# Kernel tuning notes

Measured on AMD Instinct MI355X. Metric: run time of the kernel, lower is better.

## Reference

```python
import jax, jax.numpy as jnp
import numpy as np

B, L, D, N, K = 4, 4096, 1024, 64, 3
EPS = 1e-6

def setup_inputs() -> dict:
    key = jax.random.key(0)
    ks = jax.random.split(key, 24)
    f32 = jnp.float32
    inp = {
        'T': jax.random.normal(ks[0], (B, L, D), f32),
        'norm_scale': jnp.ones((D,), f32),
        'in_w': jax.random.normal(ks[1], (2 * D, D), f32) * (1.0 / np.sqrt(D)),
        'in_b': jnp.zeros((2 * D,), f32),
        'dw_w': jax.random.normal(ks[2], (D, 1, K), f32) * (1.0 / np.sqrt(K)),
        'dw_b': jnp.zeros((D,), f32),
        'pw_w': jax.random.normal(ks[3], (D, D), f32) * (1.0 / np.sqrt(D)),
        'pw_b': jnp.zeros((D,), f32),
        'f_win': jax.random.normal(ks[4], (N, D), f32) * (1.0 / np.sqrt(D)),
        'f_wout': jax.random.normal(ks[5], (D, N), f32) * (1.0 / np.sqrt(N)),
        'f_logA': jax.random.normal(ks[6], (N,), f32) * 0.02,
        'f_B': jax.random.normal(ks[7], (N,), f32) * 0.02,
        'f_C': jax.random.normal(ks[8], (N,), f32) * 0.02,
        'f_logdt': jnp.array(0.0, f32),
        'b_win': jax.random.normal(ks[9], (N, D), f32) * (1.0 / np.sqrt(D)),
        'b_wout': jax.random.normal(ks[10], (D, N), f32) * (1.0 / np.sqrt(N)),
        'b_logA': jax.random.normal(ks[11], (N,), f32) * 0.02,
        'b_B': jax.random.normal(ks[12], (N,), f32) * 0.02,
        'b_C': jax.random.normal(ks[13], (N,), f32) * 0.02,
        'b_logdt': jnp.array(0.0, f32),
        'out_w': jax.random.normal(ks[14], (D, D), f32) * (1.0 / np.sqrt(D)),
        'out_b': jnp.zeros((D,), f32),
    }
    return inp

def _ssm(x, win, wout, logA, Bp, Cp, logdt):
    # ZOH discretization of diagonal SSM
    dt = jnp.exp(logdt)
    A = -jnp.exp(logA)
    Abar = jnp.exp(A * dt)
    denom = jnp.where(jnp.abs(A) < EPS, jnp.ones_like(A), A)
    frac = jnp.where(jnp.abs(A) < EPS, dt, (Abar - 1.0) / denom)
    Bbar = frac * Bp
    u = jnp.einsum('bld,nd->bln', x, win)  # (B,L,N)
    h0 = jnp.zeros((x.shape[0], win.shape[0]), x.dtype)
    def step(h, ut):
        h = h * Abar + ut * Bbar
        return h, h * Cp
    _, ys = jax.lax.scan(step, h0, jnp.swapaxes(u, 0, 1))  # (L,B,N)
    y = jnp.swapaxes(ys, 0, 1)
    return jnp.einsum('bln,dn->bld', y, wout)

def reference(T, norm_scale, in_w, in_b, dw_w, dw_b, pw_w, pw_b,
              f_win, f_wout, f_logA, f_B, f_C, f_logdt,
              b_win, b_wout, b_logA, b_B, b_C, b_logdt,
              out_w, out_b):
    # RMSNorm
    rms = jnp.sqrt(jnp.mean(T * T, axis=-1, keepdims=True) + EPS)
    Tn = T / rms * norm_scale
    # in_linear -> chunk
    xz = Tn @ in_w.T + in_b
    x, z = jnp.split(xz, 2, axis=-1)
    gate = jax.nn.sigmoid(z)
    # depthwise-separable conv1d (NCH layout)
    xc = jnp.swapaxes(x, 1, 2)  # (B,D,L)
    xc = jax.lax.conv_general_dilated(
        xc, dw_w, window_strides=(1,), padding=[(K // 2, K // 2)],
        dimension_numbers=('NCH', 'OIH', 'NCH'), feature_group_count=D)
    xc = xc + dw_b[None, :, None]
    xc = jnp.einsum('bdl,ed->bel', xc, pw_w) + pw_b[None, :, None]
    x_conv = jnp.swapaxes(xc, 1, 2)  # (B,L,D)
    # bidirectional SSM
    y_f = _ssm(x_conv, f_win, f_wout, f_logA, f_B, f_C, f_logdt)
    y_b = _ssm(jnp.flip(x_conv, axis=1), b_win, b_wout, b_logA, b_B, b_C, b_logdt)
    y_b = jnp.flip(y_b, axis=1)
    y = (y_f + y_b) * gate
    y = y @ out_w.T + out_b
    return T + y
```

## Files before the change

kernel.cpp:

```cpp
#include <hip/hip_runtime.h>
#include <cstdint>


#define L_SEQ 4096
#define D_DIM 1024
#define B_SZ 4
#define M_TOK (B_SZ * L_SEQ)
#define CHUNKS 64
#define CLEN (L_SEQ / CHUNKS)

typedef short bf16x8 __attribute__((ext_vector_type(8)));
typedef float floatx4 __attribute__((ext_vector_type(4)));

__device__ inline unsigned short f2bf(float f) {
  union { float f; unsigned int u; } v; v.f = f;
  unsigned int r = v.u + 0x7FFFu + ((v.u >> 16) & 1u);
  return (unsigned short)(r >> 16);
}
__device__ inline float bf2f(unsigned short h) {
  union { unsigned int u; float f; } v; v.u = ((unsigned int)h) << 16;
  return v.f;
}

__device__ inline void load_lds16(const unsigned short* g, unsigned short* l) {
  __builtin_amdgcn_global_load_lds(
      (const __attribute__((address_space(1))) unsigned int*)g,
      (__attribute__((address_space(3))) unsigned int*)l, 16, 0, 0);
}

__global__ __launch_bounds__(256) void rmsnorm_kernel(
    const float* __restrict__ T, const float* __restrict__ scale,
    unsigned short* __restrict__ Tn) {
  int tok = blockIdx.x;
  int t = threadIdx.x;
  const float4* row = (const float4*)(T + (size_t)tok * D_DIM);
  float4 v = row[t];
  float ss = v.x*v.x + v.y*v.y + v.z*v.z + v.w*v.w;
  #pragma unroll
  for (int off = 32; off > 0; off >>= 1) ss += __shfl_down(ss, off);
  __shared__ float part[4];
  if ((t & 63) == 0) part[t >> 6] = ss;
  __syncthreads();
  float total = part[0] + part[1] + part[2] + part[3];
  float rinv = rsqrtf(total * (1.0f / D_DIM) + 1e-6f);
  const float4* sc4 = (const float4*)scale;
  float4 s = sc4[t];
  ushort4 o;
  o.x = f2bf(v.x * rinv * s.x); o.y = f2bf(v.y * rinv * s.y);
  o.z = f2bf(v.z * rinv * s.z); o.w = f2bf(v.w * rinv * s.w);
  ((ushort4*)(Tn + (size_t)tok * D_DIM))[t] = o;
}

__global__ __launch_bounds__(256) void f2bf_vec_kernel(
    const float* __restrict__ in, unsigned short* __restrict__ out, int n4) {
  int i = blockIdx.x * 256 + threadIdx.x;
  if (i < n4) {
    float4 v = ((const float4*)in)[i];
    ushort4 o; o.x = f2bf(v.x); o.y = f2bf(v.y); o.z = f2bf(v.z); o.w = f2bf(v.w);
    ((ushort4*)out)[i] = o;
  }
}

__global__ void prepack_wy_kernel(
    const float* __restrict__ f_wout, const float* __restrict__ b_wout,
    unsigned short* __restrict__ Wy) {
  int i = blockIdx.x * blockDim.x + threadIdx.x;
  if (i < 128 * D_DIM) {
    int d = i >> 7, kk = i & 127;
    Wy[i] = f2bf((kk < 64) ? f_wout[d * 64 + kk] : b_wout[d * 64 + (kk - 64)]);
  }
}

__global__ void prepack_wu_kernel(
    const float* __restrict__ f_win, const float* __restrict__ b_win,
    unsigned short* __restrict__ Wu) {
  int i = blockIdx.x * blockDim.x + threadIdx.x;
  if (i < 128 * D_DIM) {
    int n = i >> 10, k = i & (D_DIM - 1);
    Wu[i] = f2bf((n < 64) ? f_win[n * D_DIM + k] : b_win[(n - 64) * D_DIM + k]);
  }
}

__global__ __launch_bounds__(256) void transpose_pw_kernel(
    const float* __restrict__ in, unsigned short* __restrict__ outT) {
  __shared__ float tile[32][33];
  int bd = blockIdx.x * 32, be = blockIdx.y * 32;
  int tx = threadIdx.x & 31, ty = threadIdx.x >> 5;
  #pragma unroll
  for (int j = 0; j < 32; j += 8)
    tile[ty + j][tx] = in[(size_t)(be + ty + j) * D_DIM + bd + tx];
  __syncthreads();
  #pragma unroll
  for (int j = 0; j < 32; j += 8)
    outT[(size_t)(bd + ty + j) * D_DIM + be + tx] = f2bf(tile[tx][ty + j]);
}

__global__ __launch_bounds__(64) void cbias_kernel(
    const float* __restrict__ f_win, const float* __restrict__ b_win,
    const float* __restrict__ pw_b, float* __restrict__ cb) {
  int n = blockIdx.x, t = threadIdx.x;
  const float* wrow = (n < 64) ? (f_win + (size_t)n * D_DIM)
                               : (b_win + (size_t)(n - 64) * D_DIM);
  float s = 0.0f;
  for (int e = t; e < D_DIM; e += 64) s += wrow[e] * pw_b[e];
  #pragma unroll
  for (int off = 32; off > 0; off >>= 1) s += __shfl_down(s, off);
  if (t == 0) cb[n] = s;
}

template<int MODE, typename OUT_T>
__global__ __launch_bounds__(256) void gemm_mfma_kernel(
    const unsigned short* __restrict__ A, const unsigned short* __restrict__ Bw,
    const float* __restrict__ bias, OUT_T* __restrict__ out,
    int M, int N, int Kt,
    const void* __restrict__ aux0, unsigned short* __restrict__ aux1) {
  __shared__ unsigned short As[2][128 * 32];
  __shared__ unsigned short Bs[2][128 * 32];
  int tid = threadIdx.x;
  int wave = tid >> 6, lane = tid & 63;
  int quad = lane >> 4, lrow = lane & 15;
  int nx = N >> 7;
  int nwg = nx * (M >> 7);
  int obid = blockIdx.y * nx + blockIdx.x;
  int swz = (nwg & 7) ? obid : ((obid & 7) * (nwg >> 3) + (obid >> 3));
  int bm = (swz / nx) << 7, bn = (swz % nx) << 7;
  int wm = (wave & 1) * 64, wn = (wave >> 1) * 64;

  int r0 = tid >> 2;
  int c8 = (tid & 3) * 8;
  const unsigned short* Ag0 = A  + (size_t)(bm + r0) * Kt + c8;
  const unsigned short* Ag1 = A  + (size_t)(bm + 64 + r0) * Kt + c8;
  const unsigned short* Bg0 = Bw + (size_t)(bn + r0) * Kt + c8;
  const unsigned short* Bg1 = Bw + (size_t)(bn + 64 + r0) * Kt + c8;
  int woff = wave * 512;

  floatx4 acc[4][4] = {};
  int nt = Kt >> 5;

  load_lds16(Ag0, &As[0][0] + woff);
  load_lds16(Ag1, &As[0][0] + 2048 + woff);
  load_lds16(Bg0, &Bs[0][0] + woff);
  load_lds16(Bg1, &Bs[0][0] + 2048 + woff);
  __syncthreads();

  int cur = 0;
  for (int t = 0; t < nt; ++t) {
    if (t + 1 < nt) {
      int k0 = (t + 1) << 5;
      int nb = cur ^ 1;
      load_lds16(Ag0 + k0, &As[nb][0] + woff);
      load_lds16(Ag1 + k0, &As[nb][0] + 2048 + woff);
      load_lds16(Bg0 + k0, &Bs[nb][0] + woff);
      load_lds16(Bg1 + k0, &Bs[nb][0] + 2048 + woff);
    }
    {
      const unsigned short* Ab = &As[cur][0];
      const unsigned short* Bb = &Bs[cur][0];
      bf16x8 af[4], bfr[4];
      #pragma unroll
      for (int mi = 0; mi < 4; ++mi)
        af[mi] = *(const bf16x8*)(Ab + (wm + mi * 16 + lrow) * 32 + quad * 8);
      #pragma unroll
      for (int ni = 0; ni < 4; ++ni)
        bfr[ni] = *(const bf16x8*)(Bb + (wn + ni * 16 + lrow) * 32 + quad * 8);
      __builtin_amdgcn_s_setprio(1);
      #pragma unroll
      for (int mi = 0; mi < 4; ++mi)
        #pragma unroll
        for (int ni = 0; ni < 4; ++ni)
          acc[mi][ni] = __builtin_amdgcn_mfma_f32_16x16x32_bf16(
              af[mi], bfr[ni], acc[mi][ni], 0, 0, 0);
      __builtin_amdgcn_s_setprio(0);
    }
    if (t + 1 < nt) {
      __syncthreads();
      cur ^= 1;
    }
  }

  #pragma unroll
  for (int mi = 0; mi < 4; ++mi) {
    #pragma unroll
    for (int ni = 0; ni < 4; ++ni) {
      #pragma unroll
      for (int r = 0; r < 4; ++r) {
        int m = bm + wm + mi * 16 + quad * 4 + r;
        int n = bn + wn + ni * 16 + lrow;
        float v = acc[mi][ni][r];
        if (MODE == 0) {
          if (bias) v += bias[n];
          if (sizeof(OUT_T) == 2) out[(size_t)m * N + n] = (OUT_T)f2bf(v);
          else                    out[(size_t)m * N + n] = (OUT_T)v;
        } else if (MODE == 1) {
          if (bias) v += bias[n];
          if (n < D_DIM) ((unsigned short*)out)[(size_t)m * D_DIM + n] = f2bf(v);
          else aux1[(size_t)m * D_DIM + (n - D_DIM)] = f2bf(1.0f / (1.0f + __expf(-v)));
        } else if (MODE == 2) {
          v *= bf2f(((const unsigned short*)aux0)[(size_t)m * N + n]);
          ((unsigned short*)out)[(size_t)m * N + n] = f2bf(v);
        } else {
          if (bias) v += bias[n];
          v += ((const float*)aux0)[(size_t)m * N + n];
          ((float*)out)[(size_t)m * N + n] = v;
        }
      }
    }
  }
}

__global__ __launch_bounds__(256) void dwconv_kernel(
    const unsigned short* __restrict__ x, const float* __restrict__ w,
    const float* __restrict__ b, unsigned short* __restrict__ out) {
  size_t i8 = (size_t)blockIdx.x * 256 + threadIdx.x;
  int d8 = (int)(i8 & (D_DIM / 8 - 1));
  size_t tok = i8 >> 7;
  int l = (int)(tok & (L_SEQ - 1));
  int d0 = d8 * 8;
  size_t base = tok * D_DIM + d0;
  bf16x8 cur = *(const bf16x8*)(x + base);
  float acc[8];
  #pragma unroll
  for (int j = 0; j < 8; ++j) {
    int d = d0 + j;
    acc[j] = b[d] + w[d * 3 + 1] * bf2f((unsigned short)cur[j]);
  }
  if (l > 0) {
    bf16x8 prv = *(const bf16x8*)(x + base - D_DIM);
    #pragma unroll
    for (int j = 0; j < 8; ++j) acc[j] += w[(d0 + j) * 3 + 0] * bf2f((unsigned short)prv[j]);
  }
  if (l < L_SEQ - 1) {
    bf16x8 nxt = *(const bf16x8*)(x + base + D_DIM);
    #pragma unroll
    for (int j = 0; j < 8; ++j) acc[j] += w[(d0 + j) * 3 + 2] * bf2f((unsigned short)nxt[j]);
  }
  bf16x8 o;
  #pragma unroll
  for (int j = 0; j < 8; ++j) o[j] = (short)f2bf(acc[j]);
  *(bf16x8*)(out + base) = o;
}

__device__ inline void ssm_params(
    int col,
    const float* f_logA, const float* f_B, const float* f_C, const float* f_logdt,
    const float* b_logA, const float* b_B, const float* b_C, const float* b_logdt,
    float& Abar, float& Bbar, float& Cc, float& Aa, float& dt) {
  int dir = col >> 6, n = col & 63;
  const float* logA  = dir ? b_logA  : f_logA;
  const float* Bp    = dir ? b_B     : f_B;
  const float* Cp    = dir ? b_C     : f_C;
  const float* logdt = dir ? b_logdt : f_logdt;
  dt = expf(logdt[0]);
  Aa = -expf(logA[n]);
  Abar = expf(Aa * dt);
  float frac = (fabsf(Aa) < 1e-6f) ? dt : (Abar - 1.0f) / Aa;
  Bbar = frac * Bp[n];
  Cc = Cp[n];
}

__global__ __launch_bounds__(128) void scan_s1_kernel(
    const float* __restrict__ u, float* __restrict__ states,
    const float* __restrict__ f_logA, const float* __restrict__ f_B,
    const float* __restrict__ f_C, const float* __restrict__ f_logdt,
    const float* __restrict__ b_logA, const float* __restrict__ b_B,
    const float* __restrict__ b_C, const float* __restrict__ b_logdt) {
  int col = threadIdx.x;
  int chunk = blockIdx.x, b = blockIdx.y;
  float Abar, Bbar, Cc, Aa, dt;
  ssm_params(col, f_logA, f_B, f_C, f_logdt, b_logA, b_B, b_C, b_logdt,
             Abar, Bbar, Cc, Aa, dt);
  size_t base = ((size_t)b * L_SEQ + (size_t)chunk * CLEN) * 128 + col;
  float h = 0.0f;
  if (col < 64) {
    for (int i0 = 0; i0 < CLEN; i0 += 8) {
      float uv[8];
      #pragma unroll
      for (int j = 0; j < 8; ++j) uv[j] = u[base + (size_t)(i0 + j) * 128];
      #pragma unroll
      for (int j = 0; j < 8; ++j) h = h * Abar + uv[j] * Bbar;
    }
  } else {
    for (int i0 = CLEN - 1; i0 >= 0; i0 -= 8) {
      float uv[8];
      #pragma unroll
      for (int j = 0; j < 8; ++j) uv[j] = u[base + (size_t)(i0 - j) * 128];
      #pragma unroll
      for (int j = 0; j < 8; ++j) h = h * Abar + uv[j] * Bbar;
    }
  }
  states[((size_t)b * CHUNKS + chunk) * 128 + col] = h;
}

__global__ __launch_bounds__(512) void scan_s2_kernel(
    const float* __restrict__ states, float* __restrict__ carries,
    const float* __restrict__ f_logA, const float* __restrict__ f_B,
    const float* __restrict__ f_C, const float* __restrict__ f_logdt,
    const float* __restrict__ b_logA, const float* __restrict__ b_B,
    const float* __restrict__ b_C, const float* __restrict__ b_logdt) {
  int tid = threadIdx.x;
  int b = tid >> 7, col = tid & 127;
  float Abar, Bbar, Cc, Aa, dt;
  ssm_params(col, f_logA, f_B, f_C, f_logdt, b_logA, b_B, b_C, b_logdt,
             Abar, Bbar, Cc, Aa, dt);
  float Ac = expf(Aa * dt * (float)CLEN);
  size_t sb = (size_t)b * CHUNKS * 128 + col;
  float cur = 0.0f;
  if (col < 64) {
    for (int c = 0; c < CHUNKS; ++c) {
      carries[sb + (size_t)c * 128] = cur;
      cur = cur * Ac + states[sb + (size_t)c * 128];
    }
  } else {
    for (int c = CHUNKS - 1; c >= 0; --c) {
      carries[sb + (size_t)c * 128] = cur;
      cur = cur * Ac + states[sb + (size_t)c * 128];
    }
  }
}

__global__ __launch_bounds__(128) void scan_s3_kernel(
    const float* __restrict__ u, const float* __restrict__ carries,
    unsigned short* __restrict__ y,
    const float* __restrict__ f_logA, const float* __restrict__ f_B,
    const float* __restrict__ f_C, const float* __restrict__ f_logdt,
    const float* __restrict__ b_logA, const float* __restrict__ b_B,
    const float* __restrict__ b_C, const float* __restrict__ b_logdt) {
  int col = threadIdx.x;
  int chunk = blockIdx.x, b = blockIdx.y;
  float Abar, Bbar, Cc, Aa, dt;
  ssm_params(col, f_logA, f_B, f_C, f_logdt, b_logA, b_B, b_C, b_logdt,
             Abar, Bbar, Cc, Aa, dt);
  size_t base = ((size_t)b * L_SEQ + (size_t)chunk * CLEN) * 128 + col;
  float h = carries[((size_t)b * CHUNKS + chunk) * 128 + col];
  if (col < 64) {
    for (int i0 = 0; i0 < CLEN; i0 += 8) {
      float uv[8];
      #pragma unroll
      for (int j = 0; j < 8; ++j) uv[j] = u[base + (size_t)(i0 + j) * 128];
      #pragma unroll
      for (int j = 0; j < 8; ++j) {
        h = h * Abar + uv[j] * Bbar;
        y[base + (size_t)(i0 + j) * 128] = f2bf(h * Cc);
      }
    }
  } else {
    for (int i0 = CLEN - 1; i0 >= 0; i0 -= 8) {
      float uv[8];
      #pragma unroll
      for (int j = 0; j < 8; ++j) uv[j] = u[base + (size_t)(i0 - j) * 128];
      #pragma unroll
      for (int j = 0; j < 8; ++j) {
        h = h * Abar + uv[j] * Bbar;
        y[base + (size_t)(i0 - j) * 128] = f2bf(h * Cc);
      }
    }
  }
}

extern "C" void kernel_launch(void* const* d_in, const int* in_sizes, int n_in,
                              void* d_out, int out_size, void* d_ws, size_t ws_size,
                              hipStream_t stream) {
  const float* T         = (const float*)d_in[0];
  const float* norm_scale= (const float*)d_in[1];
  const float* in_w      = (const float*)d_in[2];
  const float* in_b      = (const float*)d_in[3];
  const float* dw_w      = (const float*)d_in[4];
  const float* dw_b      = (const float*)d_in[5];
  const float* pw_w      = (const float*)d_in[6];
  const float* pw_b      = (const float*)d_in[7];
  const float* f_win     = (const float*)d_in[8];
  const float* f_wout    = (const float*)d_in[9];
  const float* f_logA    = (const float*)d_in[10];
  const float* f_B       = (const float*)d_in[11];
  const float* f_C       = (const float*)d_in[12];
  const float* f_logdt   = (const float*)d_in[13];
  const float* b_win     = (const float*)d_in[14];
  const float* b_wout    = (const float*)d_in[15];
  const float* b_logA    = (const float*)d_in[16];
  const float* b_B       = (const float*)d_in[17];
  const float* b_C       = (const float*)d_in[18];
  const float* b_logdt   = (const float*)d_in[19];
  const float* out_w     = (const float*)d_in[20];
  const float* out_b     = (const float*)d_in[21];
  float* out = (float*)d_out;

  char* ws = (char*)d_ws;
  const size_t MD = (size_t)M_TOK * D_DIM;
  unsigned short* gate  = (unsigned short*)ws;              ws += MD * 2;
  unsigned short* bufA  = (unsigned short*)ws;              ws += MD * 2;
  unsigned short* bufB  = (unsigned short*)ws;              ws += MD * 2;
  float*          u     = (float*)ws;                       ws += (size_t)M_TOK * 128 * 4;
  unsigned short* ybuf  = (unsigned short*)ws;              ws += (size_t)M_TOK * 128 * 2;
  unsigned short* w_in  = (unsigned short*)ws;              ws += (size_t)2 * D_DIM * D_DIM * 2;
  unsigned short* w_out = (unsigned short*)ws;              ws += (size_t)D_DIM * D_DIM * 2;
  unsigned short* pwT   = (unsigned short*)ws;              ws += (size_t)D_DIM * D_DIM * 2;
  unsigned short* Wu    = (unsigned short*)ws;              ws += (size_t)128 * D_DIM * 2;
  unsigned short* Wf    = (unsigned short*)ws;              ws += (size_t)128 * D_DIM * 2;
  unsigned short* Wy    = (unsigned short*)ws;              ws += (size_t)128 * D_DIM * 2;
  float*          cb    = (float*)ws;                       ws += 128 * 4;
  float*          states= (float*)ws;                       ws += (size_t)B_SZ * CHUNKS * 128 * 4;
  float*          carries=(float*)ws;

  f2bf_vec_kernel<<<(2 * D_DIM * D_DIM / 4 + 255) / 256, 256, 0, stream>>>(in_w, w_in, 2 * D_DIM * D_DIM / 4);
  f2bf_vec_kernel<<<(D_DIM * D_DIM / 4 + 255) / 256, 256, 0, stream>>>(out_w, w_out, D_DIM * D_DIM / 4);
  prepack_wy_kernel<<<(128 * D_DIM) / 256, 256, 0, stream>>>(f_wout, b_wout, Wy);
  prepack_wu_kernel<<<(128 * D_DIM) / 256, 256, 0, stream>>>(f_win, b_win, Wu);
  {
    dim3 g(D_DIM / 32, D_DIM / 32);
    transpose_pw_kernel<<<g, 256, 0, stream>>>(pw_w, pwT);
  }
  cbias_kernel<<<128, 64, 0, stream>>>(f_win, b_win, pw_b, cb);
  {
    dim3 g(D_DIM / 128, 1);
    gemm_mfma_kernel<0, unsigned short><<<g, 256, 0, stream>>>(
        Wu, pwT, nullptr, Wf, 128, D_DIM, D_DIM, nullptr, nullptr);
  }
  rmsnorm_kernel<<<M_TOK, 256, 0, stream>>>(T, norm_scale, bufA);
  {
    dim3 g((2 * D_DIM) / 128, M_TOK / 128);
    gemm_mfma_kernel<1, unsigned short><<<g, 256, 0, stream>>>(
        bufA, w_in, in_b, bufB, M_TOK, 2 * D_DIM, D_DIM, nullptr, gate);
  }
  dwconv_kernel<<<(MD / 8) / 256, 256, 0, stream>>>(bufB, dw_w, dw_b, bufA);
  {
    dim3 g(1, M_TOK / 128);
    gemm_mfma_kernel<0, float><<<g, 256, 0, stream>>>(
        bufA, Wf, cb, u, M_TOK, 128, D_DIM, nullptr, nullptr);
  }
  {
    dim3 g1(CHUNKS, B_SZ);
    scan_s1_kernel<<<g1, 128, 0, stream>>>(u, states, f_logA, f_B, f_C, f_logdt,
                                           b_logA, b_B, b_C, b_logdt);
    scan_s2_kernel<<<1, 512, 0, stream>>>(states, carries, f_logA, f_B, f_C, f_logdt,
                                          b_logA, b_B, b_C, b_logdt);
    scan_s3_kernel<<<g1, 128, 0, stream>>>(u, carries, ybuf, f_logA, f_B, f_C, f_logdt,
                                           b_logA, b_B, b_C, b_logdt);
  }
  {
    dim3 g(D_DIM / 128, M_TOK / 128);
    gemm_mfma_kernel<2, unsigned short><<<g, 256, 0, stream>>>(
        ybuf, Wy, nullptr, bufA, M_TOK, D_DIM, 128, gate, nullptr);
  }
  {
    dim3 g(D_DIM / 128, M_TOK / 128);
    gemm_mfma_kernel<3, float><<<g, 256, 0, stream>>>(
        bufA, w_out, out_b, out, M_TOK, D_DIM, D_DIM, T, nullptr);
  }
}
```

Baseline: 569.6 us.

## Split scan into more chunks, fully unroll chunk loops, merge weight prepack kernels

Raises the number of scan chunks per sequence from 64 to 512, so each chunk holds 8 steps. This gives the chunk-local scan kernels far more blocks, which are now fully unrolled with all loads issued up front. The carry-propagation kernel becomes longer (512 sequential steps), so it is batched with 8-wide prefetched loads to hide latency. The two weight-prepack kernels are merged into one launch. The trade-off is a longer serial pass and a larger state buffer in exchange for much more parallelism in the chunk passes.

Result: slower. 585.8 us (+2.8%).

```diff
diff --git a/kernel.cpp b/kernel.cpp
--- a/kernel.cpp
+++ b/kernel.cpp
@@ -6,7 +6,7 @@
 #define D_DIM 1024
 #define B_SZ 4
 #define M_TOK (B_SZ * L_SEQ)
-#define CHUNKS 64
+#define CHUNKS 512
 #define CLEN (L_SEQ / CHUNKS)
 
 typedef short bf16x8 __attribute__((ext_vector_type(8)));
@@ -61,23 +61,16 @@
   }
 }
 
-__global__ void prepack_wy_kernel(
+__global__ void prepack_w_kernel(
+    const float* __restrict__ f_win, const float* __restrict__ b_win,
     const float* __restrict__ f_wout, const float* __restrict__ b_wout,
-    unsigned short* __restrict__ Wy) {
-  int i = blockIdx.x * blockDim.x + threadIdx.x;
-  if (i < 128 * D_DIM) {
-    int d = i >> 7, kk = i & 127;
-    Wy[i] = f2bf((kk < 64) ? f_wout[d * 64 + kk] : b_wout[d * 64 + (kk - 64)]);
-  }
-}
-
-__global__ void prepack_wu_kernel(
-    const float* __restrict__ f_win, const float* __restrict__ b_win,
-    unsigned short* __restrict__ Wu) {
+    unsigned short* __restrict__ Wu, unsigned short* __restrict__ Wy) {
   int i = blockIdx.x * blockDim.x + threadIdx.x;
   if (i < 128 * D_DIM) {
     int n = i >> 10, k = i & (D_DIM - 1);
     Wu[i] = f2bf((n < 64) ? f_win[n * D_DIM + k] : b_win[(n - 64) * D_DIM + k]);
+    int d = i >> 7, kk = i & 127;
+    Wy[i] = f2bf((kk < 64) ? f_wout[d * 64 + kk] : b_wout[d * 64 + (kk - 64)]);
   }
 }
 
@@ -271,22 +264,17 @@
              Abar, Bbar, Cc, Aa, dt);
   size_t base = ((size_t)b * L_SEQ + (size_t)chunk * CLEN) * 128 + col;
   float h = 0.0f;
+  float uv[CLEN];
   if (col < 64) {
-    for (int i0 = 0; i0 < CLEN; i0 += 8) {
-      float uv[8];
-      #pragma unroll
-      for (int j = 0; j < 8; ++j) uv[j] = u[base + (size_t)(i0 + j) * 128];
-      #pragma unroll
-      for (int j = 0; j < 8; ++j) h = h * Abar + uv[j] * Bbar;
-    }
+    #pragma unroll
+    for (int j = 0; j < CLEN; ++j) uv[j] = u[base + (size_t)j * 128];
+    #pragma unroll
+    for (int j = 0; j < CLEN; ++j) h = h * Abar + uv[j] * Bbar;
   } else {
-    for (int i0 = CLEN - 1; i0 >= 0; i0 -= 8) {
-      float uv[8];
-      #pragma unroll
-      for (int j = 0; j < 8; ++j) uv[j] = u[base + (size_t)(i0 - j) * 128];
-      #pragma unroll
-      for (int j = 0; j < 8; ++j) h = h * Abar + uv[j] * Bbar;
-    }
+    #pragma unroll
+    for (int j = 0; j < CLEN; ++j) uv[j] = u[base + (size_t)(CLEN - 1 - j) * 128];
+    #pragma unroll
+    for (int j = 0; j < CLEN; ++j) h = h * Abar + uv[j] * Bbar;
   }
   states[((size_t)b * CHUNKS + chunk) * 128 + col] = h;
 }
@@ -306,14 +294,26 @@
   size_t sb = (size_t)b * CHUNKS * 128 + col;
   float cur = 0.0f;
   if (col < 64) {
-    for (int c = 0; c < CHUNKS; ++c) {
-      carries[sb + (size_t)c * 128] = cur;
-      cur = cur * Ac + states[sb + (size_t)c * 128];
+    for (int c0 = 0; c0 < CHUNKS; c0 += 8) {
+      float sv[8];
+      #pragma unroll
+      for (int j = 0; j < 8; ++j) sv[j] = states[sb + (size_t)(c0 + j) * 128];
+      #pragma unroll
+      for (int j = 0; j < 8; ++j) {
+        carries[sb + (size_t)(c0 + j) * 128] = cur;
+        cur = cur * Ac + sv[j];
+      }
     }
   } else {
-    for (int c = CHUNKS - 1; c >= 0; --c) {
-      carries[sb + (size_t)c * 128] = cur;
-      cur = cur * Ac + states[sb + (size_t)c * 128];
+    for (int c0 = CHUNKS - 1; c0 >= 0; c0 -= 8) {
+      float sv[8];
+      #pragma unroll
+      for (int j = 0; j < 8; ++j) sv[j] = states[sb + (size_t)(c0 - j) * 128];
+      #pragma unroll
+      for (int j = 0; j < 8; ++j) {
+        carries[sb + (size_t)(c0 - j) * 128] = cur;
+        cur = cur * Ac + sv[j];
+      }
     }
   }
 }
@@ -332,27 +332,22 @@
              Abar, Bbar, Cc, Aa, dt);
   size_t base = ((size_t)b * L_SEQ + (size_t)chunk * CLEN) * 128 + col;
   float h = carries[((size_t)b * CHUNKS + chunk) * 128 + col];
+  float uv[CLEN];
   if (col < 64) {
-    for (int i0 = 0; i0 < CLEN; i0 += 8) {
-      float uv[8];
-      #pragma unroll
-      for (int j = 0; j < 8; ++j) uv[j] = u[base + (size_t)(i0 + j) * 128];
-      #pragma unroll
-      for (int j = 0; j < 8; ++j) {
-        h = h * Abar + uv[j] * Bbar;
-        y[base + (size_t)(i0 + j) * 128] = f2bf(h * Cc);
-      }
+    #pragma unroll
+    for (int j = 0; j < CLEN; ++j) uv[j] = u[base + (size_t)j * 128];
+    #pragma unroll
+    for (int j = 0; j < CLEN; ++j) {
+      h = h * Abar + uv[j] * Bbar;
+      y[base + (size_t)j * 128] = f2bf(h * Cc);
     }
   } else {
-    for (int i0 = CLEN - 1; i0 >= 0; i0 -= 8) {
-      float uv[8];
-      #pragma unroll
-      for (int j = 0; j < 8; ++j) uv[j] = u[base + (size_t)(i0 - j) * 128];
-      #pragma unroll
-      for (int j = 0; j < 8; ++j) {
-        h = h * Abar + uv[j] * Bbar;
-        y[base + (size_t)(i0 - j) * 128] = f2bf(h * Cc);
-      }
+    #pragma unroll
+    for (int j = 0; j < CLEN; ++j) uv[j] = u[base + (size_t)(CLEN - 1 - j) * 128];
+    #pragma unroll
+    for (int j = 0; j < CLEN; ++j) {
+      h = h * Abar + uv[j] * Bbar;
+      y[base + (size_t)(CLEN - 1 - j) * 128] = f2bf(h * Cc);
     }
   }
 }
@@ -403,8 +398,7 @@
 
   f2bf_vec_kernel<<<(2 * D_DIM * D_DIM / 4 + 255) / 256, 256, 0, stream>>>(in_w, w_in, 2 * D_DIM * D_DIM / 4);
   f2bf_vec_kernel<<<(D_DIM * D_DIM / 4 + 255) / 256, 256, 0, stream>>>(out_w, w_out, D_DIM * D_DIM / 4);
-  prepack_wy_kernel<<<(128 * D_DIM) / 256, 256, 0, stream>>>(f_wout, b_wout, Wy);
-  prepack_wu_kernel<<<(128 * D_DIM) / 256, 256, 0, stream>>>(f_win, b_win, Wu);
+  prepack_w_kernel<<<(128 * D_DIM) / 256, 256, 0, stream>>>(f_win, b_win, f_wout, b_wout, Wu, Wy);
   {
     dim3 g(D_DIM / 32, D_DIM / 32);
     transpose_pw_kernel<<<g, 256, 0, stream>>>(pw_w, pwT);
```

## Split u-projection GEMM over K into two partial sums reduced in scan

Applied to the files above, without the earlier changes.

The N=128 projection GEMM (M=16384, K=1024) previously launched only 128 blocks, too few to fill the GPU. It now splits K into two halves with a dedicated double-buffered MFMA kernel, giving 256 blocks that each write a partial fp32 result. The two partials plus the bias are summed inside the scan kernels when u is read. The two weight prepack kernels are also merged into one launch. The cost is twice the u buffer memory and extra reads in both scan passes.

Result: no change. 566.4 us (-0.6%).

```diff
diff --git a/kernel.cpp b/kernel.cpp
--- a/kernel.cpp
+++ b/kernel.cpp
@@ -61,23 +61,16 @@
   }
 }
 
-__global__ void prepack_wy_kernel(
+__global__ void prepack_w_kernel(
+    const float* __restrict__ f_win, const float* __restrict__ b_win,
     const float* __restrict__ f_wout, const float* __restrict__ b_wout,
-    unsigned short* __restrict__ Wy) {
-  int i = blockIdx.x * blockDim.x + threadIdx.x;
-  if (i < 128 * D_DIM) {
-    int d = i >> 7, kk = i & 127;
-    Wy[i] = f2bf((kk < 64) ? f_wout[d * 64 + kk] : b_wout[d * 64 + (kk - 64)]);
-  }
-}
-
-__global__ void prepack_wu_kernel(
-    const float* __restrict__ f_win, const float* __restrict__ b_win,
-    unsigned short* __restrict__ Wu) {
+    unsigned short* __restrict__ Wu, unsigned short* __restrict__ Wy) {
   int i = blockIdx.x * blockDim.x + threadIdx.x;
   if (i < 128 * D_DIM) {
     int n = i >> 10, k = i & (D_DIM - 1);
     Wu[i] = f2bf((n < 64) ? f_win[n * D_DIM + k] : b_win[(n - 64) * D_DIM + k]);
+    int d = i >> 7, kk = i & 127;
+    Wy[i] = f2bf((kk < 64) ? f_wout[d * 64 + kk] : b_wout[d * 64 + (kk - 64)]);
   }
 }
 
@@ -208,6 +201,86 @@
   }
 }
 
+__global__ __launch_bounds__(256) void gemm_uproj_kernel(
+    const unsigned short* __restrict__ A, const unsigned short* __restrict__ Bw,
+    float* __restrict__ uP) {
+  __shared__ unsigned short As[2][128 * 32];
+  __shared__ unsigned short Bs[2][128 * 32];
+  int tid = threadIdx.x;
+  int wave = tid >> 6, lane = tid & 63;
+  int quad = lane >> 4, lrow = lane & 15;
+  int kh = blockIdx.x;
+  int bm = blockIdx.y * 128;
+  int wm = (wave & 1) * 64, wn = (wave >> 1) * 64;
+
+  int r0 = tid >> 2;
+  int c8 = (tid & 3) * 8;
+  int kbase = kh * 512;
+  const unsigned short* Ag0 = A  + (size_t)(bm + r0) * D_DIM + kbase + c8;
+  const unsigned short* Ag1 = A  + (size_t)(bm + 64 + r0) * D_DIM + kbase + c8;
+  const unsigned short* Bg0 = Bw + (size_t)(r0) * D_DIM + kbase + c8;
+  const unsigned short* Bg1 = Bw + (size_t)(64 + r0) * D_DIM + kbase + c8;
+  int woff = wave * 512;
+
+  floatx4 acc[4][4] = {};
+  const int nt = 512 >> 5;
+
+  load_lds16(Ag0, &As[0][0] + woff);
+  load_lds16(Ag1, &As[0][0] + 2048 + woff);
+  load_lds16(Bg0, &Bs[0][0] + woff);
+  load_lds16(Bg1, &Bs[0][0] + 2048 + woff);
+  __syncthreads();
+
+  int cur = 0;
+  for (int t = 0; t < nt; ++t) {
+    if (t + 1 < nt) {
+      int k0 = (t + 1) << 5;
+      int nb = cur ^ 1;
+      load_lds16(Ag0 + k0, &As[nb][0] + woff);
+      load_lds16(Ag1 + k0, &As[nb][0] + 2048 + woff);
+      load_lds16(Bg0 + k0, &Bs[nb][0] + woff);
+      load_lds16(Bg1 + k0, &Bs[nb][0] + 2048 + woff);
+    }
+    {
+      const unsigned short* Ab = &As[cur][0];
+      const unsigned short* Bb = &Bs[cur][0];
+      bf16x8 af[4], bfr[4];
+      #pragma unroll
+      for (int mi = 0; mi < 4; ++mi)
+        af[mi] = *(const bf16x8*)(Ab + (wm + mi * 16 + lrow) * 32 + quad * 8);
+      #pragma unroll
+      for (int ni = 0; ni < 4; ++ni)
+        bfr[ni] = *(const bf16x8*)(Bb + (wn + ni * 16 + lrow) * 32 + quad * 8);
+      __builtin_amdgcn_s_setprio(1);
+      #pragma unroll
+      for (int mi = 0; mi < 4; ++mi)
+        #pragma unroll
+        for (int ni = 0; ni < 4; ++ni)
+          acc[mi][ni] = __builtin_amdgcn_mfma_f32_16x16x32_bf16(
+              af[mi], bfr[ni], acc[mi][ni], 0, 0, 0);
+      __builtin_amdgcn_s_setprio(0);
+    }
+    if (t + 1 < nt) {
+      __syncthreads();
+      cur ^= 1;
+    }
+  }
+
+  float* o = uP + (size_t)kh * M_TOK * 128;
+  #pragma unroll
+  for (int mi = 0; mi < 4; ++mi) {
+    #pragma unroll
+    for (int ni = 0; ni < 4; ++ni) {
+      #pragma unroll
+      for (int r = 0; r < 4; ++r) {
+        int m = bm + wm + mi * 16 + quad * 4 + r;
+        int n = wn + ni * 16 + lrow;
+        o[(size_t)m * 128 + n] = acc[mi][ni][r];
+      }
+    }
+  }
+}
+
 __global__ __launch_bounds__(256) void dwconv_kernel(
     const unsigned short* __restrict__ x, const float* __restrict__ w,
     const float* __restrict__ b, unsigned short* __restrict__ out) {
@@ -259,7 +332,8 @@
 }
 
 __global__ __launch_bounds__(128) void scan_s1_kernel(
-    const float* __restrict__ u, float* __restrict__ states,
+    const float* __restrict__ u0, const float* __restrict__ u1,
+    const float* __restrict__ cb, float* __restrict__ states,
     const float* __restrict__ f_logA, const float* __restrict__ f_B,
     const float* __restrict__ f_C, const float* __restrict__ f_logdt,
     const float* __restrict__ b_logA, const float* __restrict__ b_B,
@@ -269,13 +343,17 @@
   float Abar, Bbar, Cc, Aa, dt;
   ssm_params(col, f_logA, f_B, f_C, f_logdt, b_logA, b_B, b_C, b_logdt,
              Abar, Bbar, Cc, Aa, dt);
+  float cbv = cb[col];
   size_t base = ((size_t)b * L_SEQ + (size_t)chunk * CLEN) * 128 + col;
   float h = 0.0f;
   if (col < 64) {
     for (int i0 = 0; i0 < CLEN; i0 += 8) {
       float uv[8];
       #pragma unroll
-      for (int j = 0; j < 8; ++j) uv[j] = u[base + (size_t)(i0 + j) * 128];
+      for (int j = 0; j < 8; ++j) {
+        size_t ix = base + (size_t)(i0 + j) * 128;
+        uv[j] = u0[ix] + u1[ix] + cbv;
+      }
       #pragma unroll
       for (int j = 0; j < 8; ++j) h = h * Abar + uv[j] * Bbar;
     }
@@ -283,7 +361,10 @@
     for (int i0 = CLEN - 1; i0 >= 0; i0 -= 8) {
       float uv[8];
       #pragma unroll
-      for (int j = 0; j < 8; ++j) uv[j] = u[base + (size_t)(i0 - j) * 128];
+      for (int j = 0; j < 8; ++j) {
+        size_t ix = base + (size_t)(i0 - j) * 128;
+        uv[j] = u0[ix] + u1[ix] + cbv;
+      }
       #pragma unroll
       for (int j = 0; j < 8; ++j) h = h * Abar + uv[j] * Bbar;
     }
@@ -319,7 +400,8 @@
 }
 
 __global__ __launch_bounds__(128) void scan_s3_kernel(
-    const float* __restrict__ u, const float* __restrict__ carries,
+    const float* __restrict__ u0, const float* __restrict__ u1,
+    const float* __restrict__ cb, const float* __restrict__ carries,
     unsigned short* __restrict__ y,
     const float* __restrict__ f_logA, const float* __restrict__ f_B,
     const float* __restrict__ f_C, const float* __restrict__ f_logdt,
@@ -330,13 +412,17 @@
   float Abar, Bbar, Cc, Aa, dt;
   ssm_params(col, f_logA, f_B, f_C, f_logdt, b_logA, b_B, b_C, b_logdt,
              Abar, Bbar, Cc, Aa, dt);
+  float cbv = cb[col];
   size_t base = ((size_t)b * L_SEQ + (size_t)chunk * CLEN) * 128 + col;
   float h = carries[((size_t)b * CHUNKS + chunk) * 128 + col];
   if (col < 64) {
     for (int i0 = 0; i0 < CLEN; i0 += 8) {
       float uv[8];
       #pragma unroll
-      for (int j = 0; j < 8; ++j) uv[j] = u[base + (size_t)(i0 + j) * 128];
+      for (int j = 0; j < 8; ++j) {
+        size_t ix = base + (size_t)(i0 + j) * 128;
+        uv[j] = u0[ix] + u1[ix] + cbv;
+      }
       #pragma unroll
       for (int j = 0; j < 8; ++j) {
         h = h * Abar + uv[j] * Bbar;
@@ -347,7 +433,10 @@
     for (int i0 = CLEN - 1; i0 >= 0; i0 -= 8) {
       float uv[8];
       #pragma unroll
-      for (int j = 0; j < 8; ++j) uv[j] = u[base + (size_t)(i0 - j) * 128];
+      for (int j = 0; j < 8; ++j) {
+        size_t ix = base + (size_t)(i0 - j) * 128;
+        uv[j] = u0[ix] + u1[ix] + cbv;
+      }
       #pragma unroll
       for (int j = 0; j < 8; ++j) {
         h = h * Abar + uv[j] * Bbar;
@@ -389,7 +478,7 @@
   unsigned short* gate  = (unsigned short*)ws;              ws += MD * 2;
   unsigned short* bufA  = (unsigned short*)ws;              ws += MD * 2;
   unsigned short* bufB  = (unsigned short*)ws;              ws += MD * 2;
-  float*          u     = (float*)ws;                       ws += (size_t)M_TOK * 128 * 4;
+  float*          u     = (float*)ws;                       ws += (size_t)2 * M_TOK * 128 * 4;
   unsigned short* ybuf  = (unsigned short*)ws;              ws += (size_t)M_TOK * 128 * 2;
   unsigned short* w_in  = (unsigned short*)ws;              ws += (size_t)2 * D_DIM * D_DIM * 2;
   unsigned short* w_out = (unsigned short*)ws;              ws += (size_t)D_DIM * D_DIM * 2;
@@ -400,11 +489,12 @@
   float*          cb    = (float*)ws;                       ws += 128 * 4;
   float*          states= (float*)ws;                       ws += (size_t)B_SZ * CHUNKS * 128 * 4;
   float*          carries=(float*)ws;
+  float* u0 = u;
+  float* u1 = u + (size_t)M_TOK * 128;
 
   f2bf_vec_kernel<<<(2 * D_DIM * D_DIM / 4 + 255) / 256, 256, 0, stream>>>(in_w, w_in, 2 * D_DIM * D_DIM / 4);
   f2bf_vec_kernel<<<(D_DIM * D_DIM / 4 + 255) / 256, 256, 0, stream>>>(out_w, w_out, D_DIM * D_DIM / 4);
-  prepack_wy_kernel<<<(128 * D_DIM) / 256, 256, 0, stream>>>(f_wout, b_wout, Wy);
-  prepack_wu_kernel<<<(128 * D_DIM) / 256, 256, 0, stream>>>(f_win, b_win, Wu);
+  prepack_w_kernel<<<(128 * D_DIM) / 256, 256, 0, stream>>>(f_win, b_win, f_wout, b_wout, Wu, Wy);
   {
     dim3 g(D_DIM / 32, D_DIM / 32);
     transpose_pw_kernel<<<g, 256, 0, stream>>>(pw_w, pwT);
@@ -423,17 +513,18 @@
   }
   dwconv_kernel<<<(MD / 8) / 256, 256, 0, stream>>>(bufB, dw_w, dw_b, bufA);
   {
-    dim3 g(1, M_TOK / 128);
-    gemm_mfma_kernel<0, float><<<g, 256, 0, stream>>>(
-        bufA, Wf, cb, u, M_TOK, 128, D_DIM, nullptr, nullptr);
+    dim3 g(2, M_TOK / 128);
+    gemm_uproj_kernel<<<g, 256, 0, stream>>>(bufA, Wf, u);
   }
   {
     dim3 g1(CHUNKS, B_SZ);
-    scan_s1_kernel<<<g1, 128, 0, stream>>>(u, states, f_logA, f_B, f_C, f_logdt,
+    scan_s1_kernel<<<g1, 128, 0, stream>>>(u0, u1, cb, states,
+                                           f_logA, f_B, f_C, f_logdt,
                                            b_logA, b_B, b_C, b_logdt);
     scan_s2_kernel<<<1, 512, 0, stream>>>(states, carries, f_logA, f_B, f_C, f_logdt,
                                           b_logA, b_B, b_C, b_logdt);
-    scan_s3_kernel<<<g1, 128, 0, stream>>>(u, carries, ybuf, f_logA, f_B, f_C, f_logdt,
+    scan_s3_kernel<<<g1, 128, 0, stream>>>(u0, u1, cb, carries, ybuf,
+                                           f_logA, f_B, f_C, f_logdt,
                                            b_logA, b_B, b_C, b_logdt);
   }
   {
```
